# Performance work log

Measured on AMD Instinct MI355X. Metric: run time of the kernel, lower is better.

The kernel has to match this reference:

```python
import jax, jax.numpy as jnp
import numpy as np

MAXDISP = 192
D = MAXDISP // 3  # 64 disparity levels at 1/3 resolution


def setup_inputs() -> dict:
    key = jax.random.key(0)
    k1, k2 = jax.random.split(key)
    B, C, H, W = 2, 32, 80, 240
    x = jax.random.normal(k1, (B, C, H, W), dtype=jnp.float32)  # left features
    y = jax.random.normal(k2, (B, C, H, W), dtype=jnp.float32)  # right features
    return {"x": x, "y": y}


def reference(x, y):
    # Faithful vectorization of:
    #   cost = zeros(B, 2C, D, H, W)
    #   for i in range(D):
    #       cost[:, :C, i, :, i:] = x[:, :, :, i:]
    #       cost[:, C:, i, :, i:] = y[:, :, :, :W-i]
    B, C, H, W = x.shape
    d = jnp.arange(D)                      # [D]
    w = jnp.arange(W)                      # [W]
    mask = (w[None, :] >= d[:, None]).astype(x.dtype)   # [D, W]; zero for w < disparity
    m = mask[None, None, :, None, :]                    # [1,1,D,1,W]

    # left half: x broadcast over disparity, masked
    left = x[:, :, None, :, :] * m                      # [B,C,D,H,W]

    # right half: y shifted right by d along W, masked
    idx = jnp.clip(w[None, :] - d[:, None], 0)          # [D, W]
    right = jnp.take(y, idx, axis=3)                    # [B,C,H,D,W]
    right = jnp.moveaxis(right, 3, 2) * m               # [B,C,D,H,W]

    return jnp.concatenate([left, right], axis=1)       # [B,2C,D,H,W]
```

## Files before the change

kernel.cpp:

```cpp
#include <hip/hip_runtime.h>


#define BB 2
#define CC 32
#define DD 64
#define HH 80
#define WW 240
#define W4 (WW / 4)

__global__ __launch_bounds__(256) void costvol_kernel(const float* __restrict__ x,
                                                      const float* __restrict__ y,
                                                      float* __restrict__ out,
                                                      unsigned nq) {
    unsigned q = blockIdx.x * 256u + threadIdx.x;
    if (q >= nq) return;

    unsigned qw = q % W4;
    unsigned t  = q / W4;
    unsigned h  = t % HH;        t /= HH;
    unsigned d  = t % DD;        t /= DD;
    unsigned c2 = t % (2 * CC);
    unsigned b  = t / (2 * CC);

    unsigned w0 = qw * 4u;
    float4 v;

    if (c2 < CC) {
        const float4* xr = (const float4*)(x + (size_t)((b * CC + c2) * HH + h) * WW);
        v = xr[qw];
        if (w0 + 0 < d) v.x = 0.f;
        if (w0 + 1 < d) v.y = 0.f;
        if (w0 + 2 < d) v.z = 0.f;
        if (w0 + 3 < d) v.w = 0.f;
    } else {
        unsigned c = c2 - CC;
        const float* yr = y + (size_t)((b * CC + c) * HH + h) * WW;
        v.x = (w0 + 0 >= d) ? yr[w0 + 0 - d] : 0.f;
        v.y = (w0 + 1 >= d) ? yr[w0 + 1 - d] : 0.f;
        v.z = (w0 + 2 >= d) ? yr[w0 + 2 - d] : 0.f;
        v.w = (w0 + 3 >= d) ? yr[w0 + 3 - d] : 0.f;
    }

    ((float4*)out)[q] = v;
}

extern "C" void kernel_launch(void* const* d_in, const int* in_sizes, int n_in,
                              void* d_out, int out_size, void* d_ws, size_t ws_size,
                              hipStream_t stream) {
    const float* x = (const float*)d_in[0];
    const float* y = (const float*)d_in[1];
    float* out     = (float*)d_out;

    unsigned nq = (unsigned)(out_size / 4);
    dim3 grid((nq + 255u) / 256u), block(256);
    hipLaunchKernelGGL(costvol_kernel, grid, block, 0, stream, x, y, out, nq);
}
```

Measured before the change: 678.3 us.

## Stage input rows in shared memory and emit all disparities per block

Each block now handles one (b,c,h) row. It loads the x row and a zero-padded y row into LDS once, then writes all 64 disparity slices for both the left and right halves. The old version had every output float4 index-decoded and reread from global memory, with unaligned scalar gathers for the shifted y. This cuts redundant global reads and index math, and the zero padding removes the masking branches on the right half. In exchange the grid shrinks to 5120 blocks, each issuing 30 strided stores, and the dimensions are hardcoded.

```diff
diff --git a/kernel.cpp b/kernel.cpp
--- a/kernel.cpp
+++ b/kernel.cpp
@@ -1,47 +1,63 @@
 #include <hip/hip_runtime.h>
 
 
-#define BB 2
-#define CC 32
-#define DD 64
-#define HH 80
-#define WW 240
-#define W4 (WW / 4)
+#define W4    60u
+#define CH4   307200u
+#define D4    4800u
 
 __global__ __launch_bounds__(256) void costvol_kernel(const float* __restrict__ x,
                                                       const float* __restrict__ y,
-                                                      float* __restrict__ out,
-                                                      unsigned nq) {
-    unsigned q = blockIdx.x * 256u + threadIdx.x;
-    if (q >= nq) return;
+                                                      float* __restrict__ out) {
+    __shared__ float xs[240];
+    __shared__ float ysbuf[64 + 240];
 
-    unsigned qw = q % W4;
-    unsigned t  = q / W4;
-    unsigned h  = t % HH;        t /= HH;
-    unsigned d  = t % DD;        t /= DD;
-    unsigned c2 = t % (2 * CC);
-    unsigned b  = t / (2 * CC);
+    const unsigned t  = threadIdx.x;
+    const unsigned blk = blockIdx.x;
+    const unsigned h  = blk % 80u;
+    const unsigned bc = blk / 80u;
+    const unsigned c  = bc % 32u;
+    const unsigned b  = bc / 32u;
 
-    unsigned w0 = qw * 4u;
-    float4 v;
+    const float4* xrow = (const float4*)(x + (size_t)blk * 240u);
+    const float4* yrow = (const float4*)(y + (size_t)blk * 240u);
 
-    if (c2 < CC) {
-        const float4* xr = (const float4*)(x + (size_t)((b * CC + c2) * HH + h) * WW);
-        v = xr[qw];
-        if (w0 + 0 < d) v.x = 0.f;
-        if (w0 + 1 < d) v.y = 0.f;
-        if (w0 + 2 < d) v.z = 0.f;
-        if (w0 + 3 < d) v.w = 0.f;
-    } else {
-        unsigned c = c2 - CC;
-        const float* yr = y + (size_t)((b * CC + c) * HH + h) * WW;
-        v.x = (w0 + 0 >= d) ? yr[w0 + 0 - d] : 0.f;
-        v.y = (w0 + 1 >= d) ? yr[w0 + 1 - d] : 0.f;
-        v.z = (w0 + 2 >= d) ? yr[w0 + 2 - d] : 0.f;
-        v.w = (w0 + 3 >= d) ? yr[w0 + 3 - d] : 0.f;
+    if (t < 16u)                 ((float4*)ysbuf)[t]       = make_float4(0.f, 0.f, 0.f, 0.f);
+    else if (t < 76u)            ((float4*)ysbuf)[t]       = yrow[t - 16u];
+    if (t >= 128u && t < 188u)   ((float4*)xs)[t - 128u]   = xrow[t - 128u];
+    __syncthreads();
+
+    const float* ys = ysbuf + 64;
+    float4* out4 = (float4*)out;
+    const unsigned baseL = (b * 64u + c)       * CH4 + h * W4;
+    const unsigned baseR = (b * 64u + 32u + c) * CH4 + h * W4;
+
+    #pragma unroll
+    for (unsigned it = 0; it < 15u; ++it) {
+        unsigned i  = it * 256u + t;
+        unsigned d  = i / 60u;
+        unsigned qw = i - d * 60u;
+        float4 v = ((const float4*)xs)[qw];
+        int w0 = 4 * (int)qw, dd = (int)d;
+        if (w0 + 0 < dd) v.x = 0.f;
+        if (w0 + 1 < dd) v.y = 0.f;
+        if (w0 + 2 < dd) v.z = 0.f;
+        if (w0 + 3 < dd) v.w = 0.f;
+        out4[baseL + d * D4 + qw] = v;
     }
 
-    ((float4*)out)[q] = v;
+    #pragma unroll
+    for (unsigned it = 0; it < 15u; ++it) {
+        unsigned i  = it * 256u + t;
+        unsigned d  = i / 60u;
+        unsigned qw = i - d * 60u;
+        int s = 4 * (int)qw - (int)d;
+        float4 v;
+        v.x = ys[s + 0];
+        v.y = ys[s + 1];
+        v.z = ys[s + 2];
+        v.w = ys[s + 3];
+        out4[baseR + d * D4 + qw] = v;
+    }
 }
 
 extern "C" void kernel_launch(void* const* d_in, const int* in_sizes, int n_in,
@@ -51,7 +67,6 @@
     const float* y = (const float*)d_in[1];
     float* out     = (float*)d_out;
 
-    unsigned nq = (unsigned)(out_size / 4);
-    dim3 grid((nq + 255u) / 256u), block(256);
-    hipLaunchKernelGGL(costvol_kernel, grid, block, 0, stream, x, y, out, nq);
+    dim3 grid(2u * 32u * 80u), block(256);
+    hipLaunchKernelGGL(costvol_kernel, grid, block, 0, stream, x, y, out);
 }
```

Result: faster. 653.3 us (-3.7%).
